# Kernel tuning notes

Measured on AMD Instinct MI355X. Metric: run time of the kernel, lower is better.

## Reference

```python
import jax, jax.numpy as jnp
import numpy as np


def setup_inputs() -> dict:
    key = jax.random.key(0)
    ks = jax.random.split(key, 8)
    B, Cin, Cattr, Cout, H, W = 8, 256, 256, 256, 64, 64
    x = jax.random.normal(ks[0], (B, Cin, H, W), dtype=jnp.float32)
    attr = jax.random.normal(ks[1], (B, Cattr, H, W), dtype=jnp.float32)
    # 1x1 conv weights stored as [out, in] (kernel_size=1 squeezed)
    sq = 1.0 / np.sqrt(Cin)
    sa = 1.0 / np.sqrt(Cattr)
    Wq = jax.random.uniform(ks[2], (Cout, Cin), jnp.float32, -sq, sq)
    bq = jax.random.uniform(ks[3], (Cout,), jnp.float32, -sq, sq)
    Wk = jax.random.uniform(ks[4], (Cout, Cattr), jnp.float32, -sa, sa)
    bk = jax.random.uniform(ks[5], (Cout,), jnp.float32, -sa, sa)
    Wv = jax.random.uniform(ks[6], (Cout, Cattr), jnp.float32, -sa, sa)
    bv = jax.random.uniform(ks[7], (Cout,), jnp.float32, -sa, sa)
    return {"x": x, "attr": attr, "Wq": Wq, "bq": bq, "Wk": Wk, "bk": bk, "Wv": Wv, "bv": bv}


def reference(x, attr, Wq, bq, Wk, bk, Wv, bv):
    B, Cin, H, W = x.shape
    # 1x1 convs == per-pixel linear projections
    q = jnp.einsum('bchw,oc->bohw', x, Wq) + bq[None, :, None, None]      # [B,C,H,W]
    k = jnp.einsum('bchw,oc->bohw', attr, Wk) + bk[None, :, None, None]
    v = jnp.einsum('bchw,oc->bohw', attr, Wv) + bv[None, :, None, None]
    C = q.shape[1]
    qf = q.reshape(B, C, H * W)   # [B,C,N]
    kf = k.reshape(B, C, H * W)
    vf = v.reshape(B, C, H * W)
    # attn[b,i,j] = sum_c q[b,c,i] * k[b,c,j]  -> softmax over j
    attn = jax.nn.softmax(jnp.einsum('bci,bcj->bij', qf, kf), axis=-1)    # [B,N,N]
    out = jnp.einsum('bcj,bij->bci', vf, attn)                            # [B,C,N]
    return out.reshape(B, C, H, W) + x
```

## Files before the change

### kernel.cpp

```cpp
#include <hip/hip_runtime.h>

typedef _Float16 f16;
typedef _Float16 f16x8 __attribute__((ext_vector_type(8)));
typedef _Float16 f16x4 __attribute__((ext_vector_type(4)));
typedef float f32x4 __attribute__((ext_vector_type(4)));
typedef float f32x16 __attribute__((ext_vector_type(16)));

#define LOG2E 1.44269504088896340736f
#define SOFF  36.0f
#define CDIM 256
#define NPIX 4096

__device__ __forceinline__ void gl2lds16(const f16* g, const f16* l) {
    __builtin_amdgcn_global_load_lds((const __attribute__((address_space(1))) unsigned int*)g,
                                     (__attribute__((address_space(3))) unsigned int*)l, 16, 0, 0);
}

__global__ void convert_w_kernel(const float* __restrict__ Wq, const float* __restrict__ Wk,
                                 const float* __restrict__ Wv,
                                 f16* __restrict__ Wq_h, f16* __restrict__ Wk_h,
                                 f16* __restrict__ Wv_h) {
    int i = blockIdx.x * 256 + threadIdx.x;
    Wq_h[i] = (f16)(Wq[i] * LOG2E);
    Wk_h[i] = (f16)Wk[i];
    Wv_h[i] = (f16)Wv[i];
}

__global__ __launch_bounds__(256, 2)
void proj_kernel(const float* __restrict__ x, const float* __restrict__ attr,
                 const f16* __restrict__ Wq_h, const float* __restrict__ bq,
                 const f16* __restrict__ Wk_h, const float* __restrict__ bk,
                 const f16* __restrict__ Wv_h, const float* __restrict__ bv,
                 f16* __restrict__ qT, f16* __restrict__ kT, f16* __restrict__ vW) {
    __shared__ __align__(16) f16 Xs[64 * 256];
    __shared__ __align__(16) f16 As[64 * 256];

    const int b  = blockIdx.x & 7;
    const int i0 = (blockIdx.x >> 3) * 64;
    const int t  = threadIdx.x;
    const int w = t >> 6, lane = t & 63, l31 = lane & 31, hi = lane >> 5;
    const int xorv = l31 & 7;

    {
        const int i  = t & 63;
        const int cb = t >> 6;
        const float* xb = x    + (size_t)b * CDIM * NPIX + i0 + i;
        const float* ab = attr + (size_t)b * CDIM * NPIX + i0 + i;
#pragma unroll 2
        for (int rep = 0; rep < 8; ++rep) {
            int chunk = cb * 8 + rep;
            const float* xs = xb + (size_t)(chunk * 8) * NPIX;
            const float* as_ = ab + (size_t)(chunk * 8) * NPIX;
            f16x8 xv, av;
#pragma unroll
            for (int e = 0; e < 8; ++e) {
                xv[e] = (f16)xs[(size_t)e * NPIX];
                av[e] = (f16)as_[(size_t)e * NPIX];
            }
            int phys = chunk ^ (i & 7);
            *(f16x8*)(Xs + i * 256 + phys * 8) = xv;
            *(f16x8*)(As + i * 256 + phys * 8) = av;
        }
    }
    __syncthreads();

#pragma unroll 1
    for (int k = 0; k < 12; ++k) {
        const int tt = w + 4 * k;
        const int kind = tt >> 4;
        const int rr = tt & 15;
        const int ct = rr >> 1;
        const int half = rr & 1;

        const f16* Wm = (kind == 0) ? Wq_h : ((kind == 1) ? Wk_h : Wv_h);
        const f16* Bs = (kind == 0) ? Xs : As;
        const float* bias = (kind == 0) ? bq : ((kind == 1) ? bk : bv);
        const float bscale = (kind == 0) ? LOG2E : 1.0f;

        const f16* ap = Wm + (size_t)(ct * 32 + l31) * CDIM + hi * 8;
        const f16* bp = Bs + (half * 32 + l31) * 256;

        f32x16 acc;
#pragma unroll
        for (int r = 0; r < 16; ++r) acc[r] = 0.0f;
#pragma unroll
        for (int ks = 0; ks < 16; ++ks) {
            f16x8 afr = *(const f16x8*)(ap + ks * 16);
            f16x8 bfr = *(const f16x8*)(bp + (((2 * ks + hi) ^ xorv)) * 8);
            acc = __builtin_amdgcn_mfma_f32_32x32x16_f16(afr, bfr, acc, 0, 0, 0);
        }

        const int nidx = i0 + half * 32 + l31;
        if (kind < 2) {
            f16* dst = ((kind == 0) ? qT : kT)
                       + ((size_t)b * NPIX + nidx) * CDIM + ct * 32 + 4 * hi;
#pragma unroll
            for (int g = 0; g < 4; ++g) {
                f32x4 bb = *(const f32x4*)(bias + ct * 32 + 4 * hi + 8 * g);
                f16x4 pk;
#pragma unroll
                for (int e = 0; e < 4; ++e) pk[e] = (f16)(acc[4 * g + e] + bb[e] * bscale);
                *(f16x4*)(dst + 8 * g) = pk;
            }
        } else {
            f16* dst = vW + (size_t)b * CDIM * NPIX + nidx;
#pragma unroll
            for (int g = 0; g < 4; ++g) {
                f32x4 bb = *(const f32x4*)(bias + ct * 32 + 4 * hi + 8 * g);
#pragma unroll
                for (int e = 0; e < 4; ++e) {
                    int c = ct * 32 + 4 * hi + 8 * g + e;
                    dst[(size_t)c * NPIX] = (f16)(acc[4 * g + e] + bb[e]);
                }
            }
        }
    }
}

__global__ __launch_bounds__(512, 2)
void attn_kernel(const f16* __restrict__ qT, const f16* __restrict__ kT,
                 const f16* __restrict__ vW, const float* __restrict__ x,
                 float* __restrict__ out) {
    extern __shared__ unsigned char smem[];

    const int b    = blockIdx.x & 7;
    const int i0   = (blockIdx.x >> 3) * 128;
    const int t    = threadIdx.x;
    const int w    = t >> 6;
    const int lane = t & 63;
    const int l31  = lane & 31;
    const int hi   = lane >> 5;
    const int iw   = (w & 3) * 32;
    const int jh   = (w >> 2) * 32;
    const int jh8  = (w >> 2) * 4;
    const int ig   = i0 + iw + l31;
    const int xorv = l31 & 7;

    f16x8 qf[16];
    {
        const f16* qp = qT + ((size_t)b * NPIX + ig) * CDIM + hi * 8;
#pragma unroll
        for (int ks = 0; ks < 16; ++ks) qf[ks] = *(const f16x8*)(qp + ks * 16);
    }

    int kp4o[4];
    {
        int kboff = (jh + l31) * 256 + (hi ^ (xorv & 1)) * 8;
        const int xv2 = xorv >> 1;
#pragma unroll
        for (int r = 0; r < 4; ++r) kp4o[r] = kboff + (r ^ xv2) * 16;
    }
    int vp2o[2];
    {
        int vboff = 16384 + l31 * 64;
#pragma unroll
        for (int kj = 0; kj < 2; ++kj) vp2o[kj] = vboff + (((jh8 + 2 * kj + hi) ^ xorv)) * 8;
    }

    f32x16 acc[8];
#pragma unroll
    for (int ct = 0; ct < 8; ++ct)
#pragma unroll
        for (int r = 0; r < 16; ++r) acc[ct][r] = 0.0f;
    float lrun = 0.0f;

    const f16* kb = kT + (size_t)b * NPIX * CDIM;
    const f16* vb = vW + (size_t)b * CDIM * NPIX;
    f16* lds0 = (f16*)smem;
    const int wub = (t & ~63) * 8;

    {
#pragma unroll
        for (int rep = 0; rep < 4; ++rep) {
            int slot = t + rep * 512;
            int krow = slot >> 5, kpc = slot & 31;
            gl2lds16(kb + (size_t)krow * CDIM + ((kpc ^ (krow & 7)) * 8),
                     lds0 + wub + rep * 4096);
            int vrow = slot >> 3, vpc = slot & 7;
            gl2lds16(vb + (size_t)vrow * NPIX + ((vpc ^ (vrow & 7)) * 8),
                     lds0 + 16384 + wub + rep * 4096);
        }
    }

    union Q4 { f16x4 h; unsigned int u[2]; };
    union B8 { f16x8 h; unsigned int u[4]; };

#pragma unroll 1
    for (int jt = 0; jt < 64; ++jt) {
        const int p = jt & 1;
        __syncthreads();

        if (jt < 63) {
            const int j0n = (jt + 1) * 64;
            f16* dstb = lds0 + (p ^ 1) * 32768;
#pragma unroll
            for (int rep = 0; rep < 4; ++rep) {
                int slot = t + rep * 512;
                int krow = slot >> 5, kpc = slot & 31;
                gl2lds16(kb + (size_t)(j0n + krow) * CDIM + ((kpc ^ (krow & 7)) * 8),
                         dstb + wub + rep * 4096);
                int vrow = slot >> 3, vpc = slot & 7;
                gl2lds16(vb + (size_t)vrow * NPIX + j0n + ((vpc ^ (vrow & 7)) * 8),
                         dstb + 16384 + wub + rep * 4096);
            }
        }

        const f16* L = lds0 + p * 32768;

        f32x16 s;
#pragma unroll
        for (int r = 0; r < 16; ++r) s[r] = -SOFF;
#pragma unroll
        for (int ks = 0; ks < 16; ++ks)
            s = __builtin_amdgcn_mfma_f32_32x32x16_f16(
                *(const f16x8*)(L + kp4o[ks & 3] + (ks >> 2) * 64), qf[ks], s, 0, 0, 0);

        Q4 ownq[4];
        float rtot = 0.0f;
#pragma unroll
        for (int g = 0; g < 4; ++g) {
            float p0 = __builtin_amdgcn_exp2f(s[4 * g + 0]);
            float p1 = __builtin_amdgcn_exp2f(s[4 * g + 1]);
            float p2 = __builtin_amdgcn_exp2f(s[4 * g + 2]);
            float p3 = __builtin_amdgcn_exp2f(s[4 * g + 3]);
            rtot += (p0 + p1) + (p2 + p3);
            ownq[g].h[0] = (f16)p0; ownq[g].h[1] = (f16)p1;
            ownq[g].h[2] = (f16)p2; ownq[g].h[3] = (f16)p3;
        }
        lrun += rtot;

        f16x8 pb[2];
#pragma unroll
        for (int kj = 0; kj < 2; ++kj) {
            int sidx = 2 * kj + 1 - hi;
            int oidx = 2 * kj + hi;
            unsigned int s0 = ownq[sidx].u[0], s1 = ownq[sidx].u[1];
            unsigned int r0 = (unsigned int)__shfl_xor((int)s0, 32);
            unsigned int r1 = (unsigned int)__shfl_xor((int)s1, 32);
            B8 bb;
            bb.u[0] = hi ? r0 : ownq[oidx].u[0];
            bb.u[1] = hi ? r1 : ownq[oidx].u[1];
            bb.u[2] = hi ? ownq[oidx].u[0] : r0;
            bb.u[3] = hi ? ownq[oidx].u[1] : r1;
            pb[kj] = bb.h;
        }

#pragma unroll
        for (int ct = 0; ct < 8; ++ct) {
            acc[ct] = __builtin_amdgcn_mfma_f32_32x32x16_f16(
                *(const f16x8*)(L + vp2o[0] + ct * 2048), pb[0], acc[ct], 0, 0, 0);
            acc[ct] = __builtin_amdgcn_mfma_f32_32x32x16_f16(
                *(const f16x8*)(L + vp2o[1] + ct * 2048), pb[1], acc[ct], 0, 0, 0);
        }
    }

    float lsum = lrun + __shfl_xor(lrun, 32);
    __syncthreads();
    float* Obuf = (float*)smem;
    float* Ls   = (float*)(smem + 131072);
    if (w >= 4) {
        float* ob = Obuf + (w - 4) * 8192;
#pragma unroll
        for (int ct = 0; ct < 8; ++ct)
#pragma unroll
            for (int r = 0; r < 16; ++r) {
                int c = ct * 32 + (r & 3) + 8 * (r >> 2) + 4 * hi;
                ob[c * 32 + l31] = acc[ct][r];
            }
        if (hi == 0) Ls[(w - 4) * 32 + l31] = lsum;
    }
    __syncthreads();
    if (w < 4) {
        const float ltot = lsum + Ls[w * 32 + l31];
        const float invl = 1.0f / ltot;
        const float* po = Obuf + w * 8192;
        const float* xb = x + (size_t)b * CDIM * NPIX + i0 + iw;
        float* og = out + (size_t)b * CDIM * NPIX + i0 + iw;
#pragma unroll
        for (int ct = 0; ct < 8; ++ct)
#pragma unroll
            for (int r = 0; r < 16; ++r) {
                int c = ct * 32 + (r & 3) + 8 * (r >> 2) + 4 * hi;
                size_t off = (size_t)c * NPIX + l31;
                og[off] = (acc[ct][r] + po[c * 32 + l31]) * invl + xb[off];
            }
    }
}

extern "C" void kernel_launch(void* const* d_in, const int* in_sizes, int n_in,
                              void* d_out, int out_size, void* d_ws, size_t ws_size,
                              hipStream_t stream) {
    const float* x    = (const float*)d_in[0];
    const float* attr = (const float*)d_in[1];
    const float* Wq   = (const float*)d_in[2];
    const float* bq   = (const float*)d_in[3];
    const float* Wk   = (const float*)d_in[4];
    const float* bk   = (const float*)d_in[5];
    const float* Wv   = (const float*)d_in[6];
    const float* bv   = (const float*)d_in[7];
    float* out = (float*)d_out;

    char* ws = (char*)d_ws;
    const size_t qkv_bytes = (size_t)8 * NPIX * CDIM * sizeof(f16);
    f16* qT   = (f16*)ws;
    f16* kT   = (f16*)(ws + qkv_bytes);
    f16* vW   = (f16*)(ws + 2 * qkv_bytes);
    f16* Wq_h = (f16*)(ws + 3 * qkv_bytes);
    f16* Wk_h = Wq_h + 65536;
    f16* Wv_h = Wk_h + 65536;

    (void)hipFuncSetAttribute((const void*)attn_kernel,
                              hipFuncAttributeMaxDynamicSharedMemorySize, 131584);

    convert_w_kernel<<<256, 256, 0, stream>>>(Wq, Wk, Wv, Wq_h, Wk_h, Wv_h);
    proj_kernel<<<512, 256, 0, stream>>>(x, attr, Wq_h, bq, Wk_h, bk, Wv_h, bv, qT, kT, vW);
    attn_kernel<<<256, 512, 131584, stream>>>(qT, kT, vW, x, out);
}
```

Baseline: 325.0 us.

## Store Q/K in MFMA-fragment layout and load K directly into registers

The projection kernel now writes Q and K pre-packed in the per-lane MFMA operand layout, using a lane-exchange so each lane stores one 16-byte fragment. The attention kernel then loads K fragments straight from global memory into registers each tile instead of staging them through LDS. Only V stays double-buffered in LDS, which halves shared memory use. The epilogue is split into two passes to fit the smaller LDS buffer. Per-tile K global loads are no longer overlapped through LDS prefetch, so they may expose latency, and the projection kernel drops its LDS staging in favour of strided register loads.

```diff
diff --git a/kernel.cpp b/kernel.cpp
--- a/kernel.cpp
+++ b/kernel.cpp
@@ -11,9 +11,26 @@
 #define CDIM 256
 #define NPIX 4096
 
+union Q4 { f16x4 h4; unsigned int u[2]; };
+union B8 { f16x8 h8; unsigned int u[4]; };
+
 __device__ __forceinline__ void gl2lds16(const f16* g, const f16* l) {
     __builtin_amdgcn_global_load_lds((const __attribute__((address_space(1))) unsigned int*)g,
                                      (__attribute__((address_space(3))) unsigned int*)l, 16, 0, 0);
+}
+
+__device__ __forceinline__ f16x8 quad_exchange(const Q4* oq, int ksl, int hi) {
+    int sidx = 2 * ksl + 1 - hi;
+    int oidx = 2 * ksl + hi;
+    unsigned int s0 = oq[sidx].u[0], s1 = oq[sidx].u[1];
+    unsigned int r0 = (unsigned int)__shfl_xor((int)s0, 32);
+    unsigned int r1 = (unsigned int)__shfl_xor((int)s1, 32);
+    B8 bb;
+    bb.u[0] = hi ? r0 : oq[oidx].u[0];
+    bb.u[1] = hi ? r1 : oq[oidx].u[1];
+    bb.u[2] = hi ? oq[oidx].u[0] : r0;
+    bb.u[3] = hi ? oq[oidx].u[1] : r1;
+    return bb.h8;
 }
 
 __global__ void convert_w_kernel(const float* __restrict__ Wq, const float* __restrict__ Wk,
@@ -31,82 +48,98 @@
                  const f16* __restrict__ Wq_h, const float* __restrict__ bq,
                  const f16* __restrict__ Wk_h, const float* __restrict__ bk,
                  const f16* __restrict__ Wv_h, const float* __restrict__ bv,
-                 f16* __restrict__ qT, f16* __restrict__ kT, f16* __restrict__ vW) {
-    __shared__ __align__(16) f16 Xs[64 * 256];
-    __shared__ __align__(16) f16 As[64 * 256];
-
+                 f16* __restrict__ qTf, f16* __restrict__ kTf, f16* __restrict__ vW) {
     const int b  = blockIdx.x & 7;
     const int i0 = (blockIdx.x >> 3) * 64;
     const int t  = threadIdx.x;
     const int w = t >> 6, lane = t & 63, l31 = lane & 31, hi = lane >> 5;
-    const int xorv = l31 & 7;
+    const int h  = w & 1;
+    const int cg = w >> 1;
+    const int px = i0 + 32 * h + l31;
+    const int it = (i0 >> 5) + h;
 
     {
-        const int i  = t & 63;
-        const int cb = t >> 6;
-        const float* xb = x    + (size_t)b * CDIM * NPIX + i0 + i;
-        const float* ab = attr + (size_t)b * CDIM * NPIX + i0 + i;
-#pragma unroll 2
-        for (int rep = 0; rep < 8; ++rep) {
-            int chunk = cb * 8 + rep;
-            const float* xs = xb + (size_t)(chunk * 8) * NPIX;
-            const float* as_ = ab + (size_t)(chunk * 8) * NPIX;
-            f16x8 xv, av;
-#pragma unroll
-            for (int e = 0; e < 8; ++e) {
-                xv[e] = (f16)xs[(size_t)e * NPIX];
-                av[e] = (f16)as_[(size_t)e * NPIX];
-            }
-            int phys = chunk ^ (i & 7);
-            *(f16x8*)(Xs + i * 256 + phys * 8) = xv;
-            *(f16x8*)(As + i * 256 + phys * 8) = av;
-        }
-    }
-    __syncthreads();
-
-#pragma unroll 1
-    for (int k = 0; k < 12; ++k) {
-        const int tt = w + 4 * k;
-        const int kind = tt >> 4;
-        const int rr = tt & 15;
-        const int ct = rr >> 1;
-        const int half = rr & 1;
-
-        const f16* Wm = (kind == 0) ? Wq_h : ((kind == 1) ? Wk_h : Wv_h);
-        const f16* Bs = (kind == 0) ? Xs : As;
-        const float* bias = (kind == 0) ? bq : ((kind == 1) ? bk : bv);
-        const float bscale = (kind == 0) ? LOG2E : 1.0f;
-
-        const f16* ap = Wm + (size_t)(ct * 32 + l31) * CDIM + hi * 8;
-        const f16* bp = Bs + (half * 32 + l31) * 256;
-
-        f32x16 acc;
-#pragma unroll
-        for (int r = 0; r < 16; ++r) acc[r] = 0.0f;
+        f16x8 xa[16];
+        const float* xb = x + (size_t)b * CDIM * NPIX + (size_t)(8 * hi) * NPIX + px;
 #pragma unroll
         for (int ks = 0; ks < 16; ++ks) {
-            f16x8 afr = *(const f16x8*)(ap + ks * 16);
-            f16x8 bfr = *(const f16x8*)(bp + (((2 * ks + hi) ^ xorv)) * 8);
-            acc = __builtin_amdgcn_mfma_f32_32x32x16_f16(afr, bfr, acc, 0, 0, 0);
-        }
-
-        const int nidx = i0 + half * 32 + l31;
-        if (kind < 2) {
-            f16* dst = ((kind == 0) ? qT : kT)
-                       + ((size_t)b * NPIX + nidx) * CDIM + ct * 32 + 4 * hi;
+            f16x8 v;
+#pragma unroll
+            for (int e = 0; e < 8; ++e) v[e] = (f16)xb[(size_t)(16 * ks + e) * NPIX];
+            xa[ks] = v;
+        }
+#pragma unroll 1
+        for (int c4 = 0; c4 < 4; ++c4) {
+            const int ct = cg * 4 + c4;
+            const f16* ap = Wq_h + (size_t)(ct * 32 + l31) * CDIM + 8 * hi;
+            f32x16 acc;
+#pragma unroll
+            for (int r = 0; r < 16; ++r) acc[r] = 0.0f;
+#pragma unroll
+            for (int ks = 0; ks < 16; ++ks)
+                acc = __builtin_amdgcn_mfma_f32_32x32x16_f16(*(const f16x8*)(ap + ks * 16), xa[ks], acc, 0, 0, 0);
+            Q4 oq[4];
 #pragma unroll
             for (int g = 0; g < 4; ++g) {
-                f32x4 bb = *(const f32x4*)(bias + ct * 32 + 4 * hi + 8 * g);
-                f16x4 pk;
-#pragma unroll
-                for (int e = 0; e < 4; ++e) pk[e] = (f16)(acc[4 * g + e] + bb[e] * bscale);
-                *(f16x4*)(dst + 8 * g) = pk;
-            }
-        } else {
-            f16* dst = vW + (size_t)b * CDIM * NPIX + nidx;
+                f32x4 bb = *(const f32x4*)(bq + ct * 32 + 4 * hi + 8 * g);
+#pragma unroll
+                for (int e = 0; e < 4; ++e) oq[g].h4[e] = (f16)(acc[4 * g + e] + bb[e] * LOG2E);
+            }
+#pragma unroll
+            for (int ksl = 0; ksl < 2; ++ksl) {
+                f16* dst = qTf + ((size_t)(b * 128 + it) * 16 + ct * 2 + ksl) * 512 + lane * 8;
+                *(f16x8*)dst = quad_exchange(oq, ksl, hi);
+            }
+        }
+    }
+
+    {
+        f16x8 aa[16];
+        const float* ab = attr + (size_t)b * CDIM * NPIX + (size_t)(8 * hi) * NPIX + px;
+#pragma unroll
+        for (int ks = 0; ks < 16; ++ks) {
+            f16x8 v;
+#pragma unroll
+            for (int e = 0; e < 8; ++e) v[e] = (f16)ab[(size_t)(16 * ks + e) * NPIX];
+            aa[ks] = v;
+        }
+#pragma unroll 1
+        for (int c4 = 0; c4 < 4; ++c4) {
+            const int ct = cg * 4 + c4;
+            const f16* ap = Wk_h + (size_t)(ct * 32 + l31) * CDIM + 8 * hi;
+            f32x16 acc;
+#pragma unroll
+            for (int r = 0; r < 16; ++r) acc[r] = 0.0f;
+#pragma unroll
+            for (int ks = 0; ks < 16; ++ks)
+                acc = __builtin_amdgcn_mfma_f32_32x32x16_f16(*(const f16x8*)(ap + ks * 16), aa[ks], acc, 0, 0, 0);
+            Q4 oq[4];
 #pragma unroll
             for (int g = 0; g < 4; ++g) {
-                f32x4 bb = *(const f32x4*)(bias + ct * 32 + 4 * hi + 8 * g);
+                f32x4 bb = *(const f32x4*)(bk + ct * 32 + 4 * hi + 8 * g);
+#pragma unroll
+                for (int e = 0; e < 4; ++e) oq[g].h4[e] = (f16)(acc[4 * g + e] + bb[e]);
+            }
+#pragma unroll
+            for (int ksl = 0; ksl < 2; ++ksl) {
+                f16* dst = kTf + ((size_t)(b * 128 + it) * 16 + ct * 2 + ksl) * 512 + lane * 8;
+                *(f16x8*)dst = quad_exchange(oq, ksl, hi);
+            }
+        }
+#pragma unroll 1
+        for (int c4 = 0; c4 < 4; ++c4) {
+            const int ct = cg * 4 + c4;
+            const f16* ap = Wv_h + (size_t)(ct * 32 + l31) * CDIM + 8 * hi;
+            f32x16 acc;
+#pragma unroll
+            for (int r = 0; r < 16; ++r) acc[r] = 0.0f;
+#pragma unroll
+            for (int ks = 0; ks < 16; ++ks)
+                acc = __builtin_amdgcn_mfma_f32_32x32x16_f16(*(const f16x8*)(ap + ks * 16), aa[ks], acc, 0, 0, 0);
+            f16* dst = vW + (size_t)b * CDIM * NPIX + px;
+#pragma unroll
+            for (int g = 0; g < 4; ++g) {
+                f32x4 bb = *(const f32x4*)(bv + ct * 32 + 4 * hi + 8 * g);
 #pragma unroll
                 for (int e = 0; e < 4; ++e) {
                     int c = ct * 32 + 4 * hi + 8 * g + e;
@@ -118,7 +151,7 @@
 }
 
 __global__ __launch_bounds__(512, 2)
-void attn_kernel(const f16* __restrict__ qT, const f16* __restrict__ kT,
+void attn_kernel(const f16* __restrict__ qTf, const f16* __restrict__ kTf,
                  const f16* __restrict__ vW, const float* __restrict__ x,
                  float* __restrict__ out) {
     extern __shared__ unsigned char smem[];
@@ -131,31 +164,24 @@
     const int l31  = lane & 31;
     const int hi   = lane >> 5;
     const int iw   = (w & 3) * 32;
-    const int jh   = (w >> 2) * 32;
-    const int jh8  = (w >> 2) * 4;
-    const int ig   = i0 + iw + l31;
+    const int jhw  = w >> 2;
+    const int jh8  = jhw * 4;
+    const int it_i = (i0 >> 5) + (w & 3);
     const int xorv = l31 & 7;
+
+    f16* Vs = (f16*)smem;
+    float* Ls = (float*)(smem + 65536);
 
     f16x8 qf[16];
     {
-        const f16* qp = qT + ((size_t)b * NPIX + ig) * CDIM + hi * 8;
-#pragma unroll
-        for (int ks = 0; ks < 16; ++ks) qf[ks] = *(const f16x8*)(qp + ks * 16);
-    }
-
-    int kp4o[4];
-    {
-        int kboff = (jh + l31) * 256 + (hi ^ (xorv & 1)) * 8;
-        const int xv2 = xorv >> 1;
-#pragma unroll
-        for (int r = 0; r < 4; ++r) kp4o[r] = kboff + (r ^ xv2) * 16;
-    }
+        const f16* qb = qTf + ((size_t)(b * 128 + it_i) * 16) * 512 + lane * 8;
+#pragma unroll
+        for (int ks = 0; ks < 16; ++ks) qf[ks] = *(const f16x8*)(qb + ks * 512);
+    }
+
     int vp2o[2];
-    {
-        int vboff = 16384 + l31 * 64;
-#pragma unroll
-        for (int kj = 0; kj < 2; ++kj) vp2o[kj] = vboff + (((jh8 + 2 * kj + hi) ^ xorv)) * 8;
-    }
+#pragma unroll
+    for (int kj = 0; kj < 2; ++kj) vp2o[kj] = l31 * 64 + (((jh8 + 2 * kj + hi) ^ xorv)) * 8;
 
     f32x16 acc[8];
 #pragma unroll
@@ -164,56 +190,45 @@
         for (int r = 0; r < 16; ++r) acc[ct][r] = 0.0f;
     float lrun = 0.0f;
 
-    const f16* kb = kT + (size_t)b * NPIX * CDIM;
-    const f16* vb = vW + (size_t)b * CDIM * NPIX;
-    f16* lds0 = (f16*)smem;
+    const f16* vbg = vW + (size_t)b * CDIM * NPIX;
+    const f16* kf0 = kTf + ((size_t)(b * 128 + jhw) * 16) * 512 + lane * 8;
     const int wub = (t & ~63) * 8;
 
-    {
-#pragma unroll
-        for (int rep = 0; rep < 4; ++rep) {
-            int slot = t + rep * 512;
-            int krow = slot >> 5, kpc = slot & 31;
-            gl2lds16(kb + (size_t)krow * CDIM + ((kpc ^ (krow & 7)) * 8),
-                     lds0 + wub + rep * 4096);
-            int vrow = slot >> 3, vpc = slot & 7;
-            gl2lds16(vb + (size_t)vrow * NPIX + ((vpc ^ (vrow & 7)) * 8),
-                     lds0 + 16384 + wub + rep * 4096);
-        }
-    }
-
-    union Q4 { f16x4 h; unsigned int u[2]; };
-    union B8 { f16x8 h; unsigned int u[4]; };
+#pragma unroll
+    for (int rep = 0; rep < 4; ++rep) {
+        int slot = t + rep * 512;
+        int vrow = slot >> 3, vpc = slot & 7;
+        gl2lds16(vbg + (size_t)vrow * NPIX + ((vpc ^ (vrow & 7)) * 8), Vs + wub + rep * 4096);
+    }
 
 #pragma unroll 1
     for (int jt = 0; jt < 64; ++jt) {
         const int p = jt & 1;
         __syncthreads();
 
+        const f16* kp = kf0 + (size_t)jt * 16384;
+        f16x8 kf[16];
+#pragma unroll
+        for (int ks = 0; ks < 16; ++ks) kf[ks] = *(const f16x8*)(kp + ks * 512);
+
         if (jt < 63) {
             const int j0n = (jt + 1) * 64;
-            f16* dstb = lds0 + (p ^ 1) * 32768;
+            f16* dstb = Vs + (p ^ 1) * 16384;
 #pragma unroll
             for (int rep = 0; rep < 4; ++rep) {
                 int slot = t + rep * 512;
-                int krow = slot >> 5, kpc = slot & 31;
-                gl2lds16(kb + (size_t)(j0n + krow) * CDIM + ((kpc ^ (krow & 7)) * 8),
+                int vrow = slot >> 3, vpc = slot & 7;
+                gl2lds16(vbg + (size_t)vrow * NPIX + j0n + ((vpc ^ (vrow & 7)) * 8),
                          dstb + wub + rep * 4096);
-                int vrow = slot >> 3, vpc = slot & 7;
-                gl2lds16(vb + (size_t)vrow * NPIX + j0n + ((vpc ^ (vrow & 7)) * 8),
-                         dstb + 16384 + wub + rep * 4096);
-            }
-        }
-
-        const f16* L = lds0 + p * 32768;
+            }
+        }
 
         f32x16 s;
 #pragma unroll
         for (int r = 0; r < 16; ++r) s[r] = -SOFF;
 #pragma unroll
         for (int ks = 0; ks < 16; ++ks)
-            s = __builtin_amdgcn_mfma_f32_32x32x16_f16(
-                *(const f16x8*)(L + kp4o[ks & 3] + (ks >> 2) * 64), qf[ks], s, 0, 0, 0);
+            s = __builtin_amdgcn_mfma_f32_32x32x16_f16(kf[ks], qf[ks], s, 0, 0, 0);
 
         Q4 ownq[4];
         float rtot = 0.0f;
@@ -224,66 +239,64 @@
             float p2 = __builtin_amdgcn_exp2f(s[4 * g + 2]);
             float p3 = __builtin_amdgcn_exp2f(s[4 * g + 3]);
             rtot += (p0 + p1) + (p2 + p3);
-            ownq[g].h[0] = (f16)p0; ownq[g].h[1] = (f16)p1;
-            ownq[g].h[2] = (f16)p2; ownq[g].h[3] = (f16)p3;
+            ownq[g].h4[0] = (f16)p0; ownq[g].h4[1] = (f16)p1;
+            ownq[g].h4[2] = (f16)p2; ownq[g].h4[3] = (f16)p3;
         }
         lrun += rtot;
 
-        f16x8 pb[2];
-#pragma unroll
-        for (int kj = 0; kj < 2; ++kj) {
-            int sidx = 2 * kj + 1 - hi;
-            int oidx = 2 * kj + hi;
-            unsigned int s0 = ownq[sidx].u[0], s1 = ownq[sidx].u[1];
-            unsigned int r0 = (unsigned int)__shfl_xor((int)s0, 32);
-            unsigned int r1 = (unsigned int)__shfl_xor((int)s1, 32);
-            B8 bb;
-            bb.u[0] = hi ? r0 : ownq[oidx].u[0];
-            bb.u[1] = hi ? r1 : ownq[oidx].u[1];
-            bb.u[2] = hi ? ownq[oidx].u[0] : r0;
-            bb.u[3] = hi ? ownq[oidx].u[1] : r1;
-            pb[kj] = bb.h;
-        }
-
+        f16x8 pb0 = quad_exchange(ownq, 0, hi);
+        f16x8 pb1 = quad_exchange(ownq, 1, hi);
+
+        const f16* Vp = Vs + p * 16384;
 #pragma unroll
         for (int ct = 0; ct < 8; ++ct) {
             acc[ct] = __builtin_amdgcn_mfma_f32_32x32x16_f16(
-                *(const f16x8*)(L + vp2o[0] + ct * 2048), pb[0], acc[ct], 0, 0, 0);
+                *(const f16x8*)(Vp + vp2o[0] + ct * 2048), pb0, acc[ct], 0, 0, 0);
             acc[ct] = __builtin_amdgcn_mfma_f32_32x32x16_f16(
-                *(const f16x8*)(L + vp2o[1] + ct * 2048), pb[1], acc[ct], 0, 0, 0);
+                *(const f16x8*)(Vp + vp2o[1] + ct * 2048), pb1, acc[ct], 0, 0, 0);
         }
     }
 
     float lsum = lrun + __shfl_xor(lrun, 32);
     __syncthreads();
+    if (w >= 4 && hi == 0) Ls[(w - 4) * 32 + l31] = lsum;
+    __syncthreads();
+    float invl = 0.0f;
+    if (w < 4) invl = 1.0f / (lsum + Ls[w * 32 + l31]);
+
     float* Obuf = (float*)smem;
-    float* Ls   = (float*)(smem + 131072);
-    if (w >= 4) {
-        float* ob = Obuf + (w - 4) * 8192;
-#pragma unroll
-        for (int ct = 0; ct < 8; ++ct)
-#pragma unroll
-            for (int r = 0; r < 16; ++r) {
-                int c = ct * 32 + (r & 3) + 8 * (r >> 2) + 4 * hi;
-                ob[c * 32 + l31] = acc[ct][r];
-            }
-        if (hi == 0) Ls[(w - 4) * 32 + l31] = lsum;
-    }
-    __syncthreads();
-    if (w < 4) {
-        const float ltot = lsum + Ls[w * 32 + l31];
-        const float invl = 1.0f / ltot;
-        const float* po = Obuf + w * 8192;
-        const float* xb = x + (size_t)b * CDIM * NPIX + i0 + iw;
-        float* og = out + (size_t)b * CDIM * NPIX + i0 + iw;
-#pragma unroll
-        for (int ct = 0; ct < 8; ++ct)
-#pragma unroll
-            for (int r = 0; r < 16; ++r) {
-                int c = ct * 32 + (r & 3) + 8 * (r >> 2) + 4 * hi;
-                size_t off = (size_t)c * NPIX + l31;
-                og[off] = (acc[ct][r] + po[c * 32 + l31]) * invl + xb[off];
-            }
+#pragma unroll 1
+    for (int pass = 0; pass < 2; ++pass) {
+        if (w >= 4) {
+            float* ob = Obuf + (w - 4) * 4096;
+#pragma unroll
+            for (int c4 = 0; c4 < 4; ++c4) {
+                const int ct = pass * 4 + c4;
+#pragma unroll
+                for (int r = 0; r < 16; ++r) {
+                    int cl = c4 * 32 + (r & 3) + 8 * (r >> 2) + 4 * hi;
+                    ob[cl * 32 + l31] = acc[ct][r];
+                }
+            }
+        }
+        __syncthreads();
+        if (w < 4) {
+            const float* po = Obuf + w * 4096;
+            const float* xb = x + (size_t)b * CDIM * NPIX + i0 + iw;
+            float* og = out + (size_t)b * CDIM * NPIX + i0 + iw;
+#pragma unroll
+            for (int c4 = 0; c4 < 4; ++c4) {
+                const int ct = pass * 4 + c4;
+#pragma unroll
+                for (int r = 0; r < 16; ++r) {
+                    int cl = c4 * 32 + (r & 3) + 8 * (r >> 2) + 4 * hi;
+                    int c  = ct * 32 + (r & 3) + 8 * (r >> 2) + 4 * hi;
+                    size_t off = (size_t)c * NPIX + l31;
+                    og[off] = (acc[ct][r] + po[cl * 32 + l31]) * invl + xb[off];
+                }
+            }
+        }
+        __syncthreads();
     }
 }
 
@@ -302,17 +315,17 @@
 
     char* ws = (char*)d_ws;
     const size_t qkv_bytes = (size_t)8 * NPIX * CDIM * sizeof(f16);
-    f16* qT   = (f16*)ws;
-    f16* kT   = (f16*)(ws + qkv_bytes);
+    f16* qTf  = (f16*)ws;
+    f16* kTf  = (f16*)(ws + qkv_bytes);
     f16* vW   = (f16*)(ws + 2 * qkv_bytes);
     f16* Wq_h = (f16*)(ws + 3 * qkv_bytes);
     f16* Wk_h = Wq_h + 65536;
     f16* Wv_h = Wk_h + 65536;
 
     (void)hipFuncSetAttribute((const void*)attn_kernel,
-                              hipFuncAttributeMaxDynamicSharedMemorySize, 131584);
+                              hipFuncAttributeMaxDynamicSharedMemorySize, 66048);
 
     convert_w_kernel<<<256, 256, 0, stream>>>(Wq, Wk, Wv, Wq_h, Wk_h, Wv_h);
-    proj_kernel<<<512, 256, 0, stream>>>(x, attr, Wq_h, bq, Wk_h, bk, Wv_h, bv, qT, kT, vW);
-    attn_kernel<<<256, 512, 131584, stream>>>(qT, kT, vW, x, out);
-}
+    proj_kernel<<<512, 256, 0, stream>>>(x, attr, Wq_h, bq, Wk_h, bk, Wv_h, bv, qTf, kTf, vW);
+    attn_kernel<<<256, 512, 66048, stream>>>(qTf, kTf, vW, x, out);
+}
```

Measured after the change: 1.152 ms. 3.54x slower.
